# Kernel tuning notes

Measured on AMD Instinct MI355X. Metric: run time of the kernel, lower is better.

## Reference

```python
import jax, jax.numpy as jnp
import numpy as np

N, E, D, H, ED = 50000, 800000, 128, 4, 64
C = D // H  # per-head channels
EPS = 1e-5


def setup_inputs() -> dict:
    key = jax.random.key(0)
    ks = jax.random.split(key, 16)
    s = 0.05
    return {
        "x": jax.random.normal(ks[0], (N, D), jnp.float32),
        "edge_index": jax.random.randint(ks[1], (2, E), 0, N, jnp.int64 if jax.config.jax_enable_x64 else jnp.int32),
        "edge_attr": jax.random.normal(ks[2], (E, ED), jnp.float32),
        "Wq": jax.random.normal(ks[3], (D, H * C), jnp.float32) * s,
        "bq": jnp.zeros((H * C,), jnp.float32),
        "Wk": jax.random.normal(ks[4], (D, H * C), jnp.float32) * s,
        "bk": jnp.zeros((H * C,), jnp.float32),
        "Wv": jax.random.normal(ks[5], (D, H * C), jnp.float32) * s,
        "bv": jnp.zeros((H * C,), jnp.float32),
        "We": jax.random.normal(ks[6], (ED, H * C), jnp.float32) * s,  # lin_edge, bias=False
        "Wskip": jax.random.normal(ks[7], (D, H * C), jnp.float32) * s,
        "bskip": jnp.zeros((H * C,), jnp.float32),
        "Wbeta": jax.random.normal(ks[8], (3 * H * C, 1), jnp.float32) * s,  # lin_beta, bias=False
        "gamma": jnp.ones((D,), jnp.float32),
        "beta_ln": jnp.zeros((D,), jnp.float32),
    }


def _transformer_conv(x, src, dst, edge_attr, Wq, bq, Wk, bk, Wv, bv, We, Wskip, bskip, Wbeta):
    q = (x @ Wq + bq).reshape(N, H, C)
    k = (x @ Wk + bk).reshape(N, H, C)
    v = (x @ Wv + bv).reshape(N, H, C)
    e = (edge_attr @ We).reshape(E, H, C)
    k_j = k[src] + e                     # [E,H,C]
    v_j = v[src] + e                     # [E,H,C]
    alpha = jnp.einsum("ehc,ehc->eh", q[dst], k_j) / jnp.sqrt(jnp.float32(C))
    # per-destination softmax over incoming edges
    m = jax.ops.segment_max(alpha, dst, num_segments=N)          # [N,H]
    m = jnp.where(jnp.isfinite(m), m, 0.0)
    a = jnp.exp(alpha - m[dst])
    denom = jax.ops.segment_sum(a, dst, num_segments=N)          # [N,H]
    alpha = a / jnp.where(denom > 0, denom, 1.0)[dst]
    out = jax.ops.segment_sum(alpha[:, :, None] * v_j, dst, num_segments=N)  # [N,H,C]
    out = out.reshape(N, H * C)
    # beta-gated skip (beta=True, root_weight)
    x_r = x @ Wskip + bskip
    b = jax.nn.sigmoid(jnp.concatenate([out, x_r, out - x_r], axis=-1) @ Wbeta)  # [N,1]
    return b * x_r + (1.0 - b) * out


def reference(x, edge_index, edge_attr, Wq, bq, Wk, bk, Wv, bv, We, Wskip, bskip, Wbeta, gamma, beta_ln):
    src, dst = edge_index[0], edge_index[1]
    res = _transformer_conv(x, src, dst, edge_attr, Wq, bq, Wk, bk, Wv, bv, We, Wskip, bskip, Wbeta)
    out = jax.nn.gelu(res, approximate=False) + x
    mu = jnp.mean(out, axis=-1, keepdims=True)
    var = jnp.var(out, axis=-1, keepdims=True)
    return (out - mu) * jax.lax.rsqrt(var + EPS) * gamma + beta_ln
```

## Files before the change

kernel.cpp:

```cpp
#include <hip/hip_runtime.h>
#include <math.h>

#define NN 50000
#define EE 800000

typedef __bf16 bf16x8 __attribute__((ext_vector_type(8)));
typedef float f32x4 __attribute__((ext_vector_type(4)));
typedef float f32x2 __attribute__((ext_vector_type(2)));
typedef unsigned short ushort_t;
typedef unsigned int uint_t;

__device__ inline ushort_t f2bf(float f) {
  uint_t u = __float_as_uint(f);
  uint_t r = (u + 0x7fffu + ((u >> 16) & 1u)) >> 16;
  return (ushort_t)r;
}
__device__ inline float bflo(uint_t u) { return __uint_as_float(u << 16); }
__device__ inline float bfhi(uint_t u) { return __uint_as_float(u & 0xffff0000u); }

__device__ inline uint_t pk4_fp8(float a0, float a1, float a2, float a3) {
  a0 = fminf(fmaxf(a0, -448.f), 448.f);
  a1 = fminf(fmaxf(a1, -448.f), 448.f);
  a2 = fminf(fmaxf(a2, -448.f), 448.f);
  a3 = fminf(fmaxf(a3, -448.f), 448.f);
  uint_t lo = (uint_t)__builtin_amdgcn_cvt_pk_fp8_f32(a0, a1, 0, false) & 0xFFFFu;
  uint_t hi = (uint_t)__builtin_amdgcn_cvt_pk_fp8_f32(a2, a3, 0, false) & 0xFFFFu;
  return lo | (hi << 16);
}

__device__ inline void wave_sync() {
  asm volatile("s_waitcnt lgkmcnt(0)" ::: "memory");
  __builtin_amdgcn_wave_barrier();
}

__global__ __launch_bounds__(256) void k_prepA(const float* __restrict__ Wbeta,
                                               float* __restrict__ wcomb,
                                               int* __restrict__ counts) {
  int b = blockIdx.x;
  int o = threadIdx.x;
  if (b == 0) {
    if (o < 128) {
      wcomb[o]       = Wbeta[o]       + Wbeta[256 + o];
      wcomb[128 + o] = Wbeta[128 + o] - Wbeta[256 + o];
    }
  } else {
    int i = (b - 1) * 256 + o;
    if (i < NN) counts[i] = 0;
  }
}

__global__ __launch_bounds__(256) void k_prepB(
    const float* __restrict__ Wq, const float* __restrict__ Wk,
    const float* __restrict__ Wv, const float* __restrict__ Ws,
    const float* __restrict__ bq, const float* __restrict__ bk,
    const float* __restrict__ bv, const float* __restrict__ bs,
    ushort_t* __restrict__ Wbt, float* __restrict__ bcat,
    const float* __restrict__ We, ushort_t* __restrict__ WebT,
    const int* __restrict__ ei, int* __restrict__ counts) {
  int b = blockIdx.x;
  if (b >= 288) {
    int i = (b - 288) * 256 + threadIdx.x;
    if (i < EE) atomicAdd(&counts[ei[EE + i]], 1);
    return;
  }
  if (b >= 256) {
    int i = (b - 256) * 256 + threadIdx.x;
    int c = i >> 6, k = i & 63;
    WebT[c * 64 + k] = f2bf(We[k * 128 + c]);
    return;
  }
  int i = b * 256 + threadIdx.x;
  int c = i >> 7, k = i & 127;
  float w;
  if (c < 128)      w = Wq[k * 128 + c];
  else if (c < 256) w = Wk[k * 128 + (c - 128)];
  else if (c < 384) w = Wv[k * 128 + (c - 256)];
  else              w = Ws[k * 128 + (c - 384)];
  Wbt[(size_t)c * 128 + k] = f2bf(w);
  if (i < 512) {
    float bb;
    if (i < 128)      bb = bq[i];
    else if (i < 256) bb = bk[i - 128];
    else if (i < 384) bb = bv[i - 256];
    else              bb = bs[i - 384];
    bcat[i] = bb;
  }
}

__global__ __launch_bounds__(256) void k_mm(const float* __restrict__ x,
                                            const ushort_t* __restrict__ Wbt,
                                            const float* __restrict__ bcat,
                                            float* __restrict__ nqx,
                                            ushort_t* __restrict__ kb,
                                            ushort_t* __restrict__ vb) {
  __shared__ ushort_t As[128 * 128];
  __shared__ ushort_t Bs[128 * 128];
  int t = threadIdx.x;
  int rb = blockIdx.x * 128;
  int cb = blockIdx.y * 128;

  for (int q = t; q < 2048; q += 256) {
    int r = q >> 4, j = q & 15;
    int row = rb + r;
    float4 f0 = make_float4(0.f, 0.f, 0.f, 0.f), f1 = f0;
    if (row < NN) {
      const float4* xp = (const float4*)&x[(size_t)row * 128 + j * 8];
      f0 = xp[0]; f1 = xp[1];
    }
    uint_t u0 = (uint_t)f2bf(f0.x) | ((uint_t)f2bf(f0.y) << 16);
    uint_t u1 = (uint_t)f2bf(f0.z) | ((uint_t)f2bf(f0.w) << 16);
    uint_t u2 = (uint_t)f2bf(f1.x) | ((uint_t)f2bf(f1.y) << 16);
    uint_t u3 = (uint_t)f2bf(f1.z) | ((uint_t)f2bf(f1.w) << 16);
    int e = r * 128 + ((j * 8) ^ ((r & 7) << 3));
    *(uint4*)&As[e] = make_uint4(u0, u1, u2, u3);
  }
  for (int q = t; q < 2048; q += 256) {
    int c = q >> 4, j = q & 15;
    uint4 w = *(const uint4*)&Wbt[(size_t)(cb + c) * 128 + j * 8];
    int e = c * 128 + ((j * 8) ^ ((c & 7) << 3));
    *(uint4*)&Bs[e] = w;
  }
  __syncthreads();

  int lane = t & 63;
  int wv = t >> 6;
  int wr = wv >> 1, wc = wv & 1;
  int l15 = lane & 15, l4 = lane >> 4;

  f32x4 acc[4][4];
#pragma unroll
  for (int i = 0; i < 4; ++i)
#pragma unroll
    for (int j = 0; j < 4; ++j) acc[i][j] = (f32x4){0.f, 0.f, 0.f, 0.f};

#pragma unroll
  for (int ks = 0; ks < 4; ++ks) {
    int kbv = ks * 32 + l4 * 8;
    bf16x8 af[4], bfr[4];
#pragma unroll
    for (int i = 0; i < 4; ++i) {
      int r = wr * 64 + i * 16 + l15;
      af[i] = *(const bf16x8*)&As[r * 128 + (kbv ^ ((r & 7) << 3))];
    }
#pragma unroll
    for (int j = 0; j < 4; ++j) {
      int c = wc * 64 + j * 16 + l15;
      bfr[j] = *(const bf16x8*)&Bs[c * 128 + (kbv ^ ((c & 7) << 3))];
    }
#pragma unroll
    for (int i = 0; i < 4; ++i)
#pragma unroll
      for (int j = 0; j < 4; ++j)
        acc[i][j] = __builtin_amdgcn_mfma_f32_16x16x32_bf16(af[i], bfr[j], acc[i][j], 0, 0, 0);
  }

#pragma unroll
  for (int j = 0; j < 4; ++j) {
    int colg = cb + wc * 64 + j * 16 + l15;
    float bv = bcat[colg];
#pragma unroll
    for (int i = 0; i < 4; ++i) {
#pragma unroll
      for (int reg = 0; reg < 4; ++reg) {
        int grow = rb + wr * 64 + i * 16 + l4 * 4 + reg;
        if (grow < NN) {
          float val = acc[i][j][reg] + bv;
          if (cb == 0)        nqx[(size_t)grow * 256 + colg] = val;
          else if (cb == 128) kb[(size_t)grow * 128 + (colg - 128)] = f2bf(val);
          else if (cb == 256) vb[(size_t)grow * 128 + (colg - 256)] = f2bf(val);
          else                nqx[(size_t)grow * 256 + (colg - 256)] = val;
        }
      }
    }
  }
}

__global__ __launch_bounds__(1024) void k_scan(int* __restrict__ counts, int* __restrict__ offsets) {
  __shared__ int wsum[16];
  __shared__ int s_carry;
  int4* counts4 = (int4*)counts;
  int4* offsets4 = (int4*)offsets;
  int t = threadIdx.x, lane = t & 63, w = t >> 6;
  if (t == 0) s_carry = 0;
  __syncthreads();
  for (int base = 0; base < 12500; base += 1024) {
    int idx = base + t;
    int4 v = (idx < 12500) ? counts4[idx] : make_int4(0, 0, 0, 0);
    int e1 = v.x, e2 = e1 + v.y, e3 = e2 + v.z, tot = e3 + v.w;
    int s = tot;
#pragma unroll
    for (int off = 1; off < 64; off <<= 1) {
      int u = __shfl_up(s, off);
      if (lane >= off) s += u;
    }
    if (lane == 63) wsum[w] = s;
    __syncthreads();
    if (t == 0) {
      int ex = s_carry;
#pragma unroll
      for (int i = 0; i < 16; ++i) { int tv = wsum[i]; wsum[i] = ex; ex += tv; }
      s_carry = ex;
    }
    __syncthreads();
    int be = wsum[w] + s - tot;
    if (idx < 12500) {
      int4 o = make_int4(be, be + e1, be + e2, be + e3);
      offsets4[idx] = o;
      counts4[idx] = o;
    }
    __syncthreads();
  }
  if (t == 0) offsets[NN] = s_carry;
}

__global__ __launch_bounds__(256) void k_fillw(const int* __restrict__ ei,
                                               int* __restrict__ cursors,
                                               const float* __restrict__ ea,
                                               const ushort_t* __restrict__ WebT,
                                               int2* __restrict__ pairs,
                                               unsigned char* __restrict__ eaW) {
  __shared__ ushort_t As[64 * 64];
  __shared__ ushort_t Bs[128 * 64];
  int t = threadIdx.x;
  int eb = blockIdx.x * 64;

  if (t < 64) {
    int e = eb + t;
    int d = ei[EE + e];
    int p = atomicAdd(&cursors[d], 1);
    pairs[p] = make_int2(e, ei[e]);
  }
  for (int q = t; q < 512; q += 256) {
    int r = q >> 3, j = q & 7;
    const float4* xp = (const float4*)&ea[(size_t)(eb + r) * 64 + j * 8];
    float4 f0 = xp[0], f1 = xp[1];
    uint_t u0 = (uint_t)f2bf(f0.x) | ((uint_t)f2bf(f0.y) << 16);
    uint_t u1 = (uint_t)f2bf(f0.z) | ((uint_t)f2bf(f0.w) << 16);
    uint_t u2 = (uint_t)f2bf(f1.x) | ((uint_t)f2bf(f1.y) << 16);
    uint_t u3 = (uint_t)f2bf(f1.z) | ((uint_t)f2bf(f1.w) << 16);
    *(uint4*)&As[r * 64 + ((j * 8) ^ ((r & 7) << 3))] = make_uint4(u0, u1, u2, u3);
  }
  for (int q = t; q < 1024; q += 256) {
    int c = q >> 3, j = q & 7;
    uint4 w = *(const uint4*)&WebT[(size_t)c * 64 + j * 8];
    *(uint4*)&Bs[c * 64 + ((j * 8) ^ ((c & 7) << 3))] = w;
  }
  __syncthreads();

  int lane = t & 63, wv = t >> 6;
  int l15 = lane & 15, l4 = lane >> 4;
  int edge = wv * 16 + l15;

  bf16x8 bfr[2];
#pragma unroll
  for (int ks = 0; ks < 2; ++ks) {
    int kbv = ks * 32 + l4 * 8;
    bfr[ks] = *(const bf16x8*)&As[edge * 64 + (kbv ^ ((edge & 7) << 3))];
  }

  f32x4 acc[8];
#pragma unroll
  for (int i = 0; i < 8; ++i) acc[i] = (f32x4){0.f, 0.f, 0.f, 0.f};

#pragma unroll
  for (int ks = 0; ks < 2; ++ks) {
    int kbv = ks * 32 + l4 * 8;
#pragma unroll
    for (int i = 0; i < 8; ++i) {
      int c = i * 16 + l15;
      bf16x8 af = *(const bf16x8*)&Bs[c * 64 + (kbv ^ ((c & 7) << 3))];
      acc[i] = __builtin_amdgcn_mfma_f32_16x16x32_bf16(af, bfr[ks], acc[i], 0, 0, 0);
    }
  }

  wave_sync();
  uint_t* dst32 = (uint_t*)As;
#pragma unroll
  for (int i = 0; i < 8; ++i)
    dst32[edge * 32 + ((i * 4 + l4) ^ ((edge & 7) << 2))] =
        pk4_fp8(acc[i][0], acc[i][1], acc[i][2], acc[i][3]);
  wave_sync();

  {
    int row = t >> 2;
    int sw = (row & 7) << 2;
    const uint_t* src32 = (const uint_t*)As + row * 32;
    int w0 = ((t & 3) * 8) ^ sw;
    int w1 = ((t & 3) * 8 + 4) ^ sw;
    uint4 lo = *(const uint4*)&src32[w0];
    uint4 hi = *(const uint4*)&src32[w1];
    unsigned char* dst = eaW + (size_t)(eb + row) * 128 + (t & 3) * 32;
    *(uint4*)dst = lo;
    *(uint4*)(dst + 16) = hi;
  }
}

__global__ __launch_bounds__(256) void k_attn(
    const float* __restrict__ nqx,
    const ushort_t* __restrict__ kb, const ushort_t* __restrict__ vb,
    const unsigned char* __restrict__ eaW,
    const int* __restrict__ offsets, const int2* __restrict__ pairs,
    const float* __restrict__ x, const float* __restrict__ wcomb,
    const float* __restrict__ gamma, const float* __restrict__ beta_ln,
    float* __restrict__ out) {
  __shared__ float sQ[4][128];
  __shared__ unsigned char sEA[4][16][144];
  __shared__ float sA[4][64];
  __shared__ int   sS[4][16];

  int t = threadIdx.x, wv = t >> 6, l = t & 63;
  int n = blockIdx.x * 4 + wv;
  int h = l >> 4, m = l & 15;
  int c0 = 2 * l, c1 = c0 + 1;
  const float scale = 0.17677669529663687f;

  const float* nrow = nqx + (size_t)n * 256;
  float2 q2 = *(const float2*)&nrow[c0];
  *(float2*)&sQ[wv][c0] = make_float2(q2.x * scale, q2.y * scale);
  if (l < 16) sS[wv][l] = 0;

  int js = offsets[n], je = offsets[n + 1];
  float acc0 = 0.f, acc1 = 0.f, lsum = 0.f;

  for (int base = js; base < je; base += 16) {
    int nj = je - base; if (nj > 16) nj = 16;
    wave_sync();

    uint4 e0 = {0,0,0,0}, e1 = {0,0,0,0};
    uint4 k0 = {0,0,0,0}, k1 = {0,0,0,0}, k2 = {0,0,0,0}, k3 = {0,0,0,0};
    if (m < nj) {
      int2 pr = pairs[base + m];
      const uint4* erow = (const uint4*)(eaW + (size_t)pr.x * 128 + 32 * h);
      e0 = erow[0]; e1 = erow[1];
      const uint4* krow = (const uint4*)(kb + (size_t)pr.y * 128 + 32 * h);
      k0 = krow[0]; k1 = krow[1]; k2 = krow[2]; k3 = krow[3];
      if (h == 0) sS[wv][m] = pr.y;
    }
    *(uint4*)&sEA[wv][m][32 * h]      = e0;
    *(uint4*)&sEA[wv][m][32 * h + 16] = e1;
    wave_sync();

    float z = 0.f;
    {
      const float* qp = &sQ[wv][32 * h];
      uint_t eu[8] = {e0.x, e0.y, e0.z, e0.w, e1.x, e1.y, e1.z, e1.w};
      uint_t ku[16] = {k0.x, k0.y, k0.z, k0.w, k1.x, k1.y, k1.z, k1.w,
                       k2.x, k2.y, k2.z, k2.w, k3.x, k3.y, k3.z, k3.w};
#pragma unroll
      for (int u = 0; u < 8; ++u) {
        f32x2 elo = __builtin_amdgcn_cvt_pk_f32_fp8(eu[u] & 0xFFFFu, false);
        f32x2 ehi = __builtin_amdgcn_cvt_pk_f32_fp8(eu[u] >> 16, false);
        float4 q4 = *(const float4*)&qp[4 * u];
        z += q4.x * (bflo(ku[2 * u]) + elo.x)
           + q4.y * (bfhi(ku[2 * u]) + elo.y)
           + q4.z * (bflo(ku[2 * u + 1]) + ehi.x)
           + q4.w * (bfhi(ku[2 * u + 1]) + ehi.y);
      }
    }
    float a = (m < nj) ? __expf(z) : 0.0f;
    lsum += a;
    sA[wv][l] = a;
    wave_sync();

    {
      int4 s0 = *(const int4*)&sS[wv][0];
      int4 s1 = *(const int4*)&sS[wv][4];
      f32x4 a0 = *(const f32x4*)&sA[wv][16 * h];
      f32x4 a1 = *(const f32x4*)&sA[wv][16 * h + 4];
      uint_t vv[8];
      int sidx[8] = {s0.x, s0.y, s0.z, s0.w, s1.x, s1.y, s1.z, s1.w};
#pragma unroll
      for (int e = 0; e < 8; ++e)
        vv[e] = *(const uint_t*)(vb + (size_t)sidx[e] * 128 + c0);
#pragma unroll
      for (int e = 0; e < 8; ++e) {
        float ae = (e < 4) ? a0[e] : a1[e - 4];
        uint_t ew = (uint_t)*(const ushort_t*)&sEA[wv][e][2 * l];
        f32x2 ef = __builtin_amdgcn_cvt_pk_f32_fp8(ew, false);
        acc0 += ae * (bflo(vv[e]) + ef.x);
        acc1 += ae * (bfhi(vv[e]) + ef.y);
      }
    }
    if (nj > 8) {
      int4 s2 = *(const int4*)&sS[wv][8];
      int4 s3 = *(const int4*)&sS[wv][12];
      f32x4 a2 = *(const f32x4*)&sA[wv][16 * h + 8];
      f32x4 a3 = *(const f32x4*)&sA[wv][16 * h + 12];
      uint_t vv[8];
      int sidx[8] = {s2.x, s2.y, s2.z, s2.w, s3.x, s3.y, s3.z, s3.w};
#pragma unroll
      for (int e = 0; e < 8; ++e)
        vv[e] = *(const uint_t*)(vb + (size_t)sidx[e] * 128 + c0);
#pragma unroll
      for (int e = 0; e < 8; ++e) {
        float ae = (e < 4) ? a2[e] : a3[e - 4];
        uint_t ew = (uint_t)*(const ushort_t*)&sEA[wv][8 + e][2 * l];
        f32x2 ef = __builtin_amdgcn_cvt_pk_f32_fp8(ew, false);
        acc0 += ae * (bflo(vv[e]) + ef.x);
        acc1 += ae * (bfhi(vv[e]) + ef.y);
      }
    }
  }

  lsum += __shfl_xor(lsum, 1); lsum += __shfl_xor(lsum, 2);
  lsum += __shfl_xor(lsum, 4); lsum += __shfl_xor(lsum, 8);

  float inv = (lsum > 0.f) ? (1.0f / lsum) : 1.0f;
  float o0 = acc0 * inv;
  float o1 = acc1 * inv;

  float2 xrv = *(const float2*)&nrow[128 + c0];
  float bp = o0 * wcomb[c0] + o1 * wcomb[c1] + xrv.x * wcomb[128 + c0] + xrv.y * wcomb[128 + c1];
#pragma unroll
  for (int off = 32; off > 0; off >>= 1) bp += __shfl_xor(bp, off);
  float bgate = 1.0f / (1.0f + __expf(-bp));
  float r0 = bgate * xrv.x + (1.0f - bgate) * o0;
  float r1 = bgate * xrv.y + (1.0f - bgate) * o1;

  float2 xv = *(const float2*)&x[(size_t)n * 128 + c0];
  float ge0 = 0.5f * r0 * (1.0f + erff(r0 * 0.70710678118654752f)) + xv.x;
  float ge1 = 0.5f * r1 * (1.0f + erff(r1 * 0.70710678118654752f)) + xv.y;

  float s1 = ge0 + ge1;
  float s2 = ge0 * ge0 + ge1 * ge1;
#pragma unroll
  for (int off = 32; off > 0; off >>= 1) {
    s1 += __shfl_xor(s1, off);
    s2 += __shfl_xor(s2, off);
  }
  float mean = s1 * (1.0f / 128.0f);
  float var = s2 * (1.0f / 128.0f) - mean * mean;
  float rstd = rsqrtf(var + 1e-5f);
  float2 ov;
  ov.x = (ge0 - mean) * rstd * gamma[c0] + beta_ln[c0];
  ov.y = (ge1 - mean) * rstd * gamma[c1] + beta_ln[c1];
  *(float2*)&out[(size_t)n * 128 + c0] = ov;
}

extern "C" void kernel_launch(void* const* d_in, const int* in_sizes, int n_in,
                              void* d_out, int out_size, void* d_ws, size_t ws_size,
                              hipStream_t stream) {
  const float* x   = (const float*)d_in[0];
  const int*   ei  = (const int*)d_in[1];
  const float* ea  = (const float*)d_in[2];
  const float* Wq  = (const float*)d_in[3];
  const float* bq  = (const float*)d_in[4];
  const float* Wk  = (const float*)d_in[5];
  const float* bk  = (const float*)d_in[6];
  const float* Wv  = (const float*)d_in[7];
  const float* bv  = (const float*)d_in[8];
  const float* We  = (const float*)d_in[9];
  const float* Wsk = (const float*)d_in[10];
  const float* bsk = (const float*)d_in[11];
  const float* Wb  = (const float*)d_in[12];
  const float* gamma = (const float*)d_in[13];
  const float* beta  = (const float*)d_in[14];
  float* out = (float*)d_out;

  char* cur = (char*)d_ws;
  auto alloc = [&](size_t bytes) {
    void* p = (void*)cur;
    cur += (bytes + 255) & ~(size_t)255;
    return p;
  };
  float*         nqx     = (float*)alloc((size_t)NN * 256 * 4);
  ushort_t*      kbuf    = (ushort_t*)alloc((size_t)NN * 128 * 2);
  ushort_t*      vbuf    = (ushort_t*)alloc((size_t)NN * 128 * 2);
  unsigned char* eaW     = (unsigned char*)alloc((size_t)EE * 128);
  int2*          pairs   = (int2*)alloc((size_t)EE * 8);
  float*         wcomb   = (float*)alloc(256 * 4);
  float*         bcat    = (float*)alloc(512 * 4);
  ushort_t*      Wbt     = (ushort_t*)alloc((size_t)512 * 128 * 2);
  ushort_t*      WebT    = (ushort_t*)alloc((size_t)128 * 64 * 2);
  int*           counts  = (int*)alloc((size_t)NN * 4);
  int*           offsets = (int*)alloc((size_t)(NN + 4) * 4);

  k_prepA<<<197, 256, 0, stream>>>(Wb, wcomb, counts);
  k_prepB<<<288 + 3125, 256, 0, stream>>>(Wq, Wk, Wv, Wsk, bq, bk, bv, bsk,
                                          Wbt, bcat, We, WebT, ei, counts);
  k_mm<<<dim3(391, 4), 256, 0, stream>>>(x, Wbt, bcat, nqx, kbuf, vbuf);
  k_scan<<<1, 1024, 0, stream>>>(counts, offsets);
  k_fillw<<<12500, 256, 0, stream>>>(ei, counts, ea, WebT, pairs, eaW);
  k_attn<<<12500, 256, 0, stream>>>(nqx, kbuf, vbuf, eaW, offsets, pairs,
                                    x, wcomb, gamma, beta, out);
}
```

Baseline: 321.2 us.

## Move edge-feature projection into attention kernel via per-chunk MFMA

The edge projection (edge_attr @ We) is no longer precomputed into a per-edge fp8 buffer. The fill kernel now only converts edge_attr to bf16, and the attention kernel runs the 64x128 projection with MFMA on each 16-edge chunk. Within a wave the result is staged in shared memory with a new index mapping. This removes the earlier fill kernel's MFMA work and keeps the gather at 128 bytes per edge, at the cost of loading We into shared memory in every attention block and doing extra MFMA work per chunk in the latency-bound gather loop.

```diff
diff --git a/kernel.cpp b/kernel.cpp
--- a/kernel.cpp
+++ b/kernel.cpp
@@ -32,6 +32,8 @@
   asm volatile("s_waitcnt lgkmcnt(0)" ::: "memory");
   __builtin_amdgcn_wave_barrier();
 }
+
+union UB8 { uint4 u; bf16x8 v; };
 
 __global__ __launch_bounds__(256) void k_prepA(const float* __restrict__ Wbeta,
                                                float* __restrict__ wcomb,
@@ -213,96 +215,45 @@
   if (t == 0) offsets[NN] = s_carry;
 }
 
-__global__ __launch_bounds__(256) void k_fillw(const int* __restrict__ ei,
-                                               int* __restrict__ cursors,
-                                               const float* __restrict__ ea,
-                                               const ushort_t* __restrict__ WebT,
-                                               int2* __restrict__ pairs,
-                                               unsigned char* __restrict__ eaW) {
-  __shared__ ushort_t As[64 * 64];
-  __shared__ ushort_t Bs[128 * 64];
+__global__ __launch_bounds__(256) void k_fill(const int* __restrict__ ei,
+                                              int* __restrict__ cursors,
+                                              const float* __restrict__ ea,
+                                              int2* __restrict__ pairs,
+                                              ushort_t* __restrict__ eab) {
   int t = threadIdx.x;
-  int eb = blockIdx.x * 64;
-
-  if (t < 64) {
-    int e = eb + t;
-    int d = ei[EE + e];
-    int p = atomicAdd(&cursors[d], 1);
-    pairs[p] = make_int2(e, ei[e]);
-  }
-  for (int q = t; q < 512; q += 256) {
-    int r = q >> 3, j = q & 7;
-    const float4* xp = (const float4*)&ea[(size_t)(eb + r) * 64 + j * 8];
-    float4 f0 = xp[0], f1 = xp[1];
-    uint_t u0 = (uint_t)f2bf(f0.x) | ((uint_t)f2bf(f0.y) << 16);
-    uint_t u1 = (uint_t)f2bf(f0.z) | ((uint_t)f2bf(f0.w) << 16);
-    uint_t u2 = (uint_t)f2bf(f1.x) | ((uint_t)f2bf(f1.y) << 16);
-    uint_t u3 = (uint_t)f2bf(f1.z) | ((uint_t)f2bf(f1.w) << 16);
-    *(uint4*)&As[r * 64 + ((j * 8) ^ ((r & 7) << 3))] = make_uint4(u0, u1, u2, u3);
-  }
-  for (int q = t; q < 1024; q += 256) {
-    int c = q >> 3, j = q & 7;
-    uint4 w = *(const uint4*)&WebT[(size_t)c * 64 + j * 8];
-    *(uint4*)&Bs[c * 64 + ((j * 8) ^ ((c & 7) << 3))] = w;
-  }
-  __syncthreads();
-
-  int lane = t & 63, wv = t >> 6;
-  int l15 = lane & 15, l4 = lane >> 4;
-  int edge = wv * 16 + l15;
-
-  bf16x8 bfr[2];
-#pragma unroll
-  for (int ks = 0; ks < 2; ++ks) {
-    int kbv = ks * 32 + l4 * 8;
-    bfr[ks] = *(const bf16x8*)&As[edge * 64 + (kbv ^ ((edge & 7) << 3))];
-  }
-
-  f32x4 acc[8];
-#pragma unroll
-  for (int i = 0; i < 8; ++i) acc[i] = (f32x4){0.f, 0.f, 0.f, 0.f};
-
-#pragma unroll
-  for (int ks = 0; ks < 2; ++ks) {
-    int kbv = ks * 32 + l4 * 8;
-#pragma unroll
-    for (int i = 0; i < 8; ++i) {
-      int c = i * 16 + l15;
-      bf16x8 af = *(const bf16x8*)&Bs[c * 64 + (kbv ^ ((c & 7) << 3))];
-      acc[i] = __builtin_amdgcn_mfma_f32_16x16x32_bf16(af, bfr[ks], acc[i], 0, 0, 0);
-    }
-  }
-
-  wave_sync();
-  uint_t* dst32 = (uint_t*)As;
-#pragma unroll
-  for (int i = 0; i < 8; ++i)
-    dst32[edge * 32 + ((i * 4 + l4) ^ ((edge & 7) << 2))] =
-        pk4_fp8(acc[i][0], acc[i][1], acc[i][2], acc[i][3]);
-  wave_sync();
-
-  {
-    int row = t >> 2;
-    int sw = (row & 7) << 2;
-    const uint_t* src32 = (const uint_t*)As + row * 32;
-    int w0 = ((t & 3) * 8) ^ sw;
-    int w1 = ((t & 3) * 8 + 4) ^ sw;
-    uint4 lo = *(const uint4*)&src32[w0];
-    uint4 hi = *(const uint4*)&src32[w1];
-    unsigned char* dst = eaW + (size_t)(eb + row) * 128 + (t & 3) * 32;
-    *(uint4*)dst = lo;
-    *(uint4*)(dst + 16) = hi;
-  }
+  int lane = t & 63;
+  int e = blockIdx.x * 64 + (t >> 2);
+  int qt = t & 3;
+  int d = ei[EE + e];
+  int p = 0;
+  if (qt == 0) p = atomicAdd(&cursors[d], 1);
+  p = __shfl(p, lane & ~3);
+  if (qt == 0) pairs[p] = make_int2(e, ei[e]);
+  const float4* src4 = (const float4*)(ea + (size_t)e * 64 + qt * 16);
+  float4 f0 = src4[0], f1 = src4[1], f2 = src4[2], f3 = src4[3];
+  uint4 o0, o1;
+  o0.x = (uint_t)f2bf(f0.x) | ((uint_t)f2bf(f0.y) << 16);
+  o0.y = (uint_t)f2bf(f0.z) | ((uint_t)f2bf(f0.w) << 16);
+  o0.z = (uint_t)f2bf(f1.x) | ((uint_t)f2bf(f1.y) << 16);
+  o0.w = (uint_t)f2bf(f1.z) | ((uint_t)f2bf(f1.w) << 16);
+  o1.x = (uint_t)f2bf(f2.x) | ((uint_t)f2bf(f2.y) << 16);
+  o1.y = (uint_t)f2bf(f2.z) | ((uint_t)f2bf(f2.w) << 16);
+  o1.z = (uint_t)f2bf(f3.x) | ((uint_t)f2bf(f3.y) << 16);
+  o1.w = (uint_t)f2bf(f3.z) | ((uint_t)f2bf(f3.w) << 16);
+  ushort_t* dst = eab + (size_t)e * 64 + qt * 16;
+  *(uint4*)dst = o0;
+  *((uint4*)dst + 1) = o1;
 }
 
 __global__ __launch_bounds__(256) void k_attn(
     const float* __restrict__ nqx,
     const ushort_t* __restrict__ kb, const ushort_t* __restrict__ vb,
-    const unsigned char* __restrict__ eaW,
+    const ushort_t* __restrict__ eab, const ushort_t* __restrict__ WebT,
     const int* __restrict__ offsets, const int2* __restrict__ pairs,
     const float* __restrict__ x, const float* __restrict__ wcomb,
     const float* __restrict__ gamma, const float* __restrict__ beta_ln,
     float* __restrict__ out) {
+  __shared__ ushort_t sWeb[128 * 64];
   __shared__ float sQ[4][128];
   __shared__ unsigned char sEA[4][16][144];
   __shared__ float sA[4][64];
@@ -314,47 +265,80 @@
   int c0 = 2 * l, c1 = c0 + 1;
   const float scale = 0.17677669529663687f;
 
+  for (int q = t; q < 1024; q += 256) {
+    int c = q >> 3, j = q & 7;
+    uint4 w = *(const uint4*)&WebT[(size_t)c * 64 + j * 8];
+    *(uint4*)&sWeb[c * 64 + ((j * 8) ^ ((c & 7) << 3))] = w;
+  }
   const float* nrow = nqx + (size_t)n * 256;
   float2 q2 = *(const float2*)&nrow[c0];
   *(float2*)&sQ[wv][c0] = make_float2(q2.x * scale, q2.y * scale);
   if (l < 16) sS[wv][l] = 0;
+  __syncthreads();
 
   int js = offsets[n], je = offsets[n + 1];
   float acc0 = 0.f, acc1 = 0.f, lsum = 0.f;
+
+  const int ebyte = (((c0 >> 4) * 4) + ((c0 >> 2) & 3)) * 4 + (c0 & 3);
 
   for (int base = js; base < je; base += 16) {
     int nj = je - base; if (nj > 16) nj = 16;
     wave_sync();
 
-    uint4 e0 = {0,0,0,0}, e1 = {0,0,0,0};
+    bf16x8 bfr0, bfr1;
+    { UB8 z; z.u = make_uint4(0, 0, 0, 0); bfr0 = z.v; bfr1 = z.v; }
     uint4 k0 = {0,0,0,0}, k1 = {0,0,0,0}, k2 = {0,0,0,0}, k3 = {0,0,0,0};
     if (m < nj) {
       int2 pr = pairs[base + m];
-      const uint4* erow = (const uint4*)(eaW + (size_t)pr.x * 128 + 32 * h);
-      e0 = erow[0]; e1 = erow[1];
+      bfr0 = *(const bf16x8*)&eab[(size_t)pr.x * 64 + h * 8];
+      bfr1 = *(const bf16x8*)&eab[(size_t)pr.x * 64 + 32 + h * 8];
       const uint4* krow = (const uint4*)(kb + (size_t)pr.y * 128 + 32 * h);
       k0 = krow[0]; k1 = krow[1]; k2 = krow[2]; k3 = krow[3];
       if (h == 0) sS[wv][m] = pr.y;
     }
-    *(uint4*)&sEA[wv][m][32 * h]      = e0;
-    *(uint4*)&sEA[wv][m][32 * h + 16] = e1;
+
+    f32x4 eacc[8];
+#pragma unroll
+    for (int i = 0; i < 8; ++i) eacc[i] = (f32x4){0.f, 0.f, 0.f, 0.f};
+#pragma unroll
+    for (int ks = 0; ks < 2; ++ks) {
+      int kbv = ks * 32 + h * 8;
+#pragma unroll
+      for (int i = 0; i < 8; ++i) {
+        int c = i * 16 + m;
+        bf16x8 af = *(const bf16x8*)&sWeb[c * 64 + (kbv ^ ((c & 7) << 3))];
+        eacc[i] = __builtin_amdgcn_mfma_f32_16x16x32_bf16(af, ks ? bfr1 : bfr0,
+                                                          eacc[i], 0, 0, 0);
+      }
+    }
+    {
+      uint_t* dst = (uint_t*)&sEA[wv][0][0];
+#pragma unroll
+      for (int i = 0; i < 8; ++i)
+        dst[m * 36 + i * 4 + h] = pk4_fp8(eacc[i][0], eacc[i][1], eacc[i][2], eacc[i][3]);
+    }
     wave_sync();
 
     float z = 0.f;
     {
       const float* qp = &sQ[wv][32 * h];
-      uint_t eu[8] = {e0.x, e0.y, e0.z, e0.w, e1.x, e1.y, e1.z, e1.w};
+      const uint_t* erow = (const uint_t*)&sEA[wv][m][0];
+      uint4 ea0 = *(const uint4*)&erow[8 * h];
+      uint4 ea1 = *(const uint4*)&erow[8 * h + 4];
+      uint_t eu[8] = {ea0.x, ea0.y, ea0.z, ea0.w, ea1.x, ea1.y, ea1.z, ea1.w};
       uint_t ku[16] = {k0.x, k0.y, k0.z, k0.w, k1.x, k1.y, k1.z, k1.w,
                        k2.x, k2.y, k2.z, k2.w, k3.x, k3.y, k3.z, k3.w};
 #pragma unroll
       for (int u = 0; u < 8; ++u) {
         f32x2 elo = __builtin_amdgcn_cvt_pk_f32_fp8(eu[u] & 0xFFFFu, false);
         f32x2 ehi = __builtin_amdgcn_cvt_pk_f32_fp8(eu[u] >> 16, false);
-        float4 q4 = *(const float4*)&qp[4 * u];
-        z += q4.x * (bflo(ku[2 * u]) + elo.x)
-           + q4.y * (bfhi(ku[2 * u]) + elo.y)
-           + q4.z * (bflo(ku[2 * u + 1]) + ehi.x)
-           + q4.w * (bfhi(ku[2 * u + 1]) + ehi.y);
+        const int qo = (u >> 2) * 16 + (u & 3) * 4;
+        const int kw = (u >> 2) * 8 + (u & 3) * 2;
+        float4 q4 = *(const float4*)&qp[qo];
+        z += q4.x * (bflo(ku[kw]) + elo.x)
+           + q4.y * (bfhi(ku[kw]) + elo.y)
+           + q4.z * (bflo(ku[kw + 1]) + ehi.x)
+           + q4.w * (bfhi(ku[kw + 1]) + ehi.y);
       }
     }
     float a = (m < nj) ? __expf(z) : 0.0f;
@@ -375,7 +359,7 @@
 #pragma unroll
       for (int e = 0; e < 8; ++e) {
         float ae = (e < 4) ? a0[e] : a1[e - 4];
-        uint_t ew = (uint_t)*(const ushort_t*)&sEA[wv][e][2 * l];
+        uint_t ew = (uint_t)*(const ushort_t*)&sEA[wv][e][ebyte];
         f32x2 ef = __builtin_amdgcn_cvt_pk_f32_fp8(ew, false);
         acc0 += ae * (bflo(vv[e]) + ef.x);
         acc1 += ae * (bfhi(vv[e]) + ef.y);
@@ -394,7 +378,7 @@
 #pragma unroll
       for (int e = 0; e < 8; ++e) {
         float ae = (e < 4) ? a2[e] : a3[e - 4];
-        uint_t ew = (uint_t)*(const ushort_t*)&sEA[wv][8 + e][2 * l];
+        uint_t ew = (uint_t)*(const ushort_t*)&sEA[wv][8 + e][ebyte];
         f32x2 ef = __builtin_amdgcn_cvt_pk_f32_fp8(ew, false);
         acc0 += ae * (bflo(vv[e]) + ef.x);
         acc1 += ae * (bfhi(vv[e]) + ef.y);
@@ -466,7 +450,7 @@
   float*         nqx     = (float*)alloc((size_t)NN * 256 * 4);
   ushort_t*      kbuf    = (ushort_t*)alloc((size_t)NN * 128 * 2);
   ushort_t*      vbuf    = (ushort_t*)alloc((size_t)NN * 128 * 2);
-  unsigned char* eaW     = (unsigned char*)alloc((size_t)EE * 128);
+  ushort_t*      eab     = (ushort_t*)alloc((size_t)EE * 64 * 2);
   int2*          pairs   = (int2*)alloc((size_t)EE * 8);
   float*         wcomb   = (float*)alloc(256 * 4);
   float*         bcat    = (float*)alloc(512 * 4);
@@ -480,7 +464,7 @@
                                           Wbt, bcat, We, WebT, ei, counts);
   k_mm<<<dim3(391, 4), 256, 0, stream>>>(x, Wbt, bcat, nqx, kbuf, vbuf);
   k_scan<<<1, 1024, 0, stream>>>(counts, offsets);
-  k_fillw<<<12500, 256, 0, stream>>>(ei, counts, ea, WebT, pairs, eaW);
-  k_attn<<<12500, 256, 0, stream>>>(nqx, kbuf, vbuf, eaW, offsets, pairs,
+  k_fill<<<12500, 256, 0, stream>>>(ei, counts, ea, pairs, eab);
+  k_attn<<<12500, 256, 0, stream>>>(nqx, kbuf, vbuf, eab, WebT, offsets, pairs,
                                     x, wcomb, gamma, beta, out);
 }
```

New measurement: 358.2 us. +11.5%, slower.
